# Performance work log

Measured on AMD Instinct MI355X. Metric: run time of the kernel, lower is better.

Reference implementation:

```python
import jax, jax.numpy as jnp
import numpy as np

N = 50000
E = 600000
F_IN = 256
H = 128            # num_hidden_units * num_heads (heads=1)
C = 20             # num_classes
NEG_SLOPE = 0.2    # PyG GATConv default


def setup_inputs() -> dict:
    key = jax.random.key(0)
    ks = jax.random.split(key, 16)
    g = lambda k, shape, fan: jax.random.normal(k, shape, jnp.float32) / np.sqrt(fan)
    return {
        "x": jax.random.normal(ks[0], (N, F_IN), jnp.float32),
        "edge_index": jax.random.randint(ks[1], (2, E), 0, N, jnp.int64),
        # GATConv 1: F_IN -> H (heads=1, concat)
        "W1": g(ks[2], (F_IN, H), F_IN),
        "a_src1": g(ks[3], (H,), H),
        "a_dst1": g(ks[4], (H,), H),
        "b1": jnp.zeros((H,), jnp.float32),
        # GATConv 2: H -> H (heads=1)
        "W2": g(ks[5], (H, H), H),
        "a_src2": g(ks[6], (H,), H),
        "a_dst2": g(ks[7], (H,), H),
        "b2": jnp.zeros((H,), jnp.float32),
        # MLP head
        "Wm1": g(ks[8], (H, H), H),
        "bm1": jnp.zeros((H,), jnp.float32),
        "Wm2": g(ks[9], (H, C), H),
        "bm2": jnp.zeros((C,), jnp.float32),
    }


def gat_layer(x, W, a_src, a_dst, b, src, dst, n_nodes):
    """Single-head GATConv (PyG semantics, self-loops already in src/dst)."""
    h = x @ W                                    # [N, H]
    # edge attention logits: leaky_relu(a_src . h_j + a_dst . h_i)
    logits = jax.nn.leaky_relu((h @ a_src)[src] + (h @ a_dst)[dst], NEG_SLOPE)  # [Etot]
    # softmax over incoming edges per target node
    m = jax.ops.segment_max(logits, dst, num_segments=n_nodes)
    e = jnp.exp(logits - m[dst])
    denom = jax.ops.segment_sum(e, dst, num_segments=n_nodes)
    coef = e / denom[dst]                        # [Etot]
    out = jax.ops.segment_sum(coef[:, None] * h[src], dst, num_segments=n_nodes)
    return out + b


def reference(x, edge_index, W1, a_src1, a_dst1, b1, W2, a_src2, a_dst2, b2, Wm1, bm1, Wm2, bm2):
    n = x.shape[0]
    loops = jnp.arange(n, dtype=edge_index.dtype)
    src = jnp.concatenate([edge_index[0], loops])  # add self loops (GATConv default)
    dst = jnp.concatenate([edge_index[1], loops])
    h = gat_layer(x, W1, a_src1, a_dst1, b1, src, dst, n)
    h = jax.nn.relu(h)                            # dropout = identity at eval
    h = gat_layer(h, W2, a_src2, a_dst2, b2, src, dst, n)
    # MLP head: Linear -> (dropout) -> ReLU -> Linear -> sigmoid
    z = jax.nn.relu(h @ Wm1 + bm1)
    return jax.nn.sigmoid(z @ Wm2 + bm2)
```

## Files before the change

kernel.cpp:

```cpp
#include <hip/hip_runtime.h>
#include <math.h>

#define F_IN 256
#define HDIM 128
#define NCLS 20
#define NEG_SLOPE 0.2f
#define SCAN_CHUNK 1024

typedef float f32x4 __attribute__((ext_vector_type(4)));
typedef _Float16 f16x2 __attribute__((ext_vector_type(2)));
typedef _Float16 f16x4 __attribute__((ext_vector_type(4)));
typedef _Float16 f16x8 __attribute__((ext_vector_type(8)));

static __device__ __forceinline__ float lrelu(float x) { return x > 0.f ? x : NEG_SLOPE * x; }

__global__ void count_kernel(const int* __restrict__ ei, int E, int N, int* __restrict__ deg) {
    int e = blockIdx.x * blockDim.x + threadIdx.x;
    int Etot = E + N;
    if (e >= Etot) return;
    int d = (e < E) ? ei[E + e] : (e - E);
    atomicAdd(&deg[d], 1);
}

__global__ __launch_bounds__(256) void scan_reduce_kernel(const int* __restrict__ deg, int n,
                                                          int* __restrict__ bsums) {
    int base = blockIdx.x * SCAN_CHUNK + threadIdx.x * 4;
    int s = 0;
    if (base + 3 < n) {
        int4 v = *reinterpret_cast<const int4*>(&deg[base]);
        s = v.x + v.y + v.z + v.w;
    } else {
#pragma unroll
        for (int j = 0; j < 4; ++j) if (base + j < n) s += deg[base + j];
    }
#pragma unroll
    for (int o = 32; o > 0; o >>= 1) s += __shfl_down(s, o);
    __shared__ int ws[4];
    int lane = threadIdx.x & 63, w = threadIdx.x >> 6;
    if (lane == 0) ws[w] = s;
    __syncthreads();
    if (threadIdx.x == 0) bsums[blockIdx.x] = ws[0] + ws[1] + ws[2] + ws[3];
}

__global__ __launch_bounds__(256) void scan_bsums_kernel(int* __restrict__ bsums, int nb,
                                                         int* __restrict__ off, int n) {
    __shared__ int sh[256];
    int tid = threadIdx.x;
    int v = (tid < nb) ? bsums[tid] : 0;
    sh[tid] = v;
    __syncthreads();
    for (int d = 1; d < 256; d <<= 1) {
        int t = (tid >= d) ? sh[tid - d] : 0;
        __syncthreads();
        sh[tid] += t;
        __syncthreads();
    }
    if (tid < nb) bsums[tid] = sh[tid] - v;
    if (tid == 255) off[n] = sh[255];
}

__global__ __launch_bounds__(256) void scan_down_kernel(const int* __restrict__ deg, int n,
                                                        const int* __restrict__ bpre,
                                                        int* __restrict__ off) {
    int base = blockIdx.x * SCAN_CHUNK + threadIdx.x * 4;
    int v0 = 0, v1 = 0, v2 = 0, v3 = 0;
    if (base + 3 < n) {
        int4 t = *reinterpret_cast<const int4*>(&deg[base]);
        v0 = t.x; v1 = t.y; v2 = t.z; v3 = t.w;
    } else {
        if (base + 0 < n) v0 = deg[base + 0];
        if (base + 1 < n) v1 = deg[base + 1];
        if (base + 2 < n) v2 = deg[base + 2];
        if (base + 3 < n) v3 = deg[base + 3];
    }
    int tsum = v0 + v1 + v2 + v3;
    int lane = threadIdx.x & 63, w = threadIdx.x >> 6;
    int inc = tsum;
#pragma unroll
    for (int o = 1; o < 64; o <<= 1) {
        int t = __shfl_up(inc, o);
        if (lane >= o) inc += t;
    }
    int texc = inc - tsum;
    __shared__ int wsum[4];
    if (lane == 63) wsum[w] = inc;
    __syncthreads();
    int wpre = 0;
    for (int i = 0; i < w; ++i) wpre += wsum[i];
    int p = bpre[blockIdx.x] + wpre + texc;
    if (base + 3 < n) {
        int4 o4;
        o4.x = p; o4.y = p + v0; o4.z = p + v0 + v1; o4.w = p + v0 + v1 + v2;
        *reinterpret_cast<int4*>(&off[base]) = o4;
    } else {
        int run = p;
        if (base + 0 < n) { off[base + 0] = run; run += v0; }
        if (base + 1 < n) { off[base + 1] = run; run += v1; }
        if (base + 2 < n) { off[base + 2] = run; run += v2; }
        if (base + 3 < n) { off[base + 3] = run; }
    }
}

__global__ void scatter_kernel(const int* __restrict__ ei, int E, int N,
                               const int* __restrict__ off, int* __restrict__ cursor,
                               int* __restrict__ csr_src) {
    int e = blockIdx.x * blockDim.x + threadIdx.x;
    int Etot = E + N;
    if (e >= Etot) return;
    int s, d;
    if (e < E) { s = ei[e]; d = ei[E + e]; } else { s = d = e - E; }
    int pos = off[d] + atomicAdd(&cursor[d], 1);
    csr_src[pos] = s;
}

__global__ __launch_bounds__(64) void pack_b_kernel(const float* __restrict__ W1,
                                                    const float* __restrict__ W2,
                                                    const float* __restrict__ Wm1,
                                                    _Float16* __restrict__ p1,
                                                    _Float16* __restrict__ p2,
                                                    _Float16* __restrict__ p3) {
    int t = blockIdx.x;
    int lane = threadIdx.x;
    const float* B; _Float16* out; int r;
    if (t < 64)      { B = W1;  out = p1; r = t; }
    else if (t < 96) { B = W2;  out = p2; r = t - 64; }
    else             { B = Wm1; out = p3; r = t - 96; }
    int ks = r >> 3, cf = r & 7;
    int c  = cf * 16 + (lane & 15);
    int k0 = ks * 32 + (lane >> 4) * 8;
    size_t base = ((size_t)r * 64 + lane) * 16;
#pragma unroll
    for (int i = 0; i < 8; ++i) {
        float v = B[(size_t)(k0 + i) * 128 + c];
        _Float16 h = (_Float16)v;
        out[base + i]     = h;
        out[base + 8 + i] = (_Float16)(v - (float)h);
    }
}

template <int AFMT, int KSTEPS>
__global__ __launch_bounds__(256) void gemm_mfma_kernel(
        const void* __restrict__ Aptr, const _Float16* __restrict__ Bp,
        _Float16* __restrict__ C, int M,
        const float* __restrict__ bias, int act,
        const float* __restrict__ a_src, const float* __restrict__ a_dst,
        float* __restrict__ as_out, float* __restrict__ ad_out) {
    constexpr int K = KSTEPS * 32;
    __shared__ float sal[2][2][64];

    int tid = threadIdx.x;
    int lane = tid & 63;
    int wid = tid >> 6;
    int wr = wid >> 1, wc = wid & 1;
    int bm = blockIdx.x * 64;
    int l15 = lane & 15, l4 = lane >> 4;
    int row0 = bm + wr * 32 + l15;
    int koff = l4 * 8;

    const float*    A32 = (const float*)Aptr;
    const _Float16* A16 = (const _Float16*)Aptr;
    bool ok0 = row0 < M, ok1 = (row0 + 16) < M;
    const f16x8 zf = {0, 0, 0, 0, 0, 0, 0, 0};

    f32x4 acc[2][4];
#pragma unroll
    for (int m = 0; m < 2; ++m)
#pragma unroll
        for (int j = 0; j < 4; ++j) acc[m][j] = (f32x4){0.f, 0.f, 0.f, 0.f};

    auto loadA = [&](int ks, f16x8 a[2]) {
        int kb = ks * 32 + koff;
#pragma unroll
        for (int m = 0; m < 2; ++m) {
            int rr = row0 + m * 16;
            bool ok = m ? ok1 : ok0;
            if (AFMT == 0) {
                if (ok) {
                    const float* p = &A32[(size_t)rr * K + kb];
                    float4 u = *reinterpret_cast<const float4*>(p);
                    float4 w = *reinterpret_cast<const float4*>(p + 4);
                    f16x8 t;
                    t[0] = (_Float16)u.x; t[1] = (_Float16)u.y;
                    t[2] = (_Float16)u.z; t[3] = (_Float16)u.w;
                    t[4] = (_Float16)w.x; t[5] = (_Float16)w.y;
                    t[6] = (_Float16)w.z; t[7] = (_Float16)w.w;
                    a[m] = t;
                } else a[m] = zf;
            } else {
                a[m] = ok ? *reinterpret_cast<const f16x8*>(&A16[(size_t)rr * K + kb]) : zf;
            }
        }
    };
    auto loadB = [&](int ks, f16x8 bh[4], f16x8 bl[4]) {
#pragma unroll
        for (int j = 0; j < 4; ++j) {
            int cf = wc * 4 + j;
            const _Float16* p = Bp + (((size_t)ks * 8 + cf) * 64 + lane) * 16;
            bh[j] = *reinterpret_cast<const f16x8*>(p);
            bl[j] = *reinterpret_cast<const f16x8*>(p + 8);
        }
    };

    f16x8 a0[2], a1[2], bh0[4], bh1[4], bl0[4], bl1[4];
    loadA(0, a0); loadB(0, bh0, bl0);
#pragma unroll
    for (int ks = 0; ks < KSTEPS; ks += 2) {
        loadA(ks + 1, a1); loadB(ks + 1, bh1, bl1);
#pragma unroll
        for (int j = 0; j < 4; ++j) {
            acc[0][j] = __builtin_amdgcn_mfma_f32_16x16x32_f16(a0[0], bh0[j], acc[0][j], 0, 0, 0);
            acc[1][j] = __builtin_amdgcn_mfma_f32_16x16x32_f16(a0[1], bh0[j], acc[1][j], 0, 0, 0);
            acc[0][j] = __builtin_amdgcn_mfma_f32_16x16x32_f16(a0[0], bl0[j], acc[0][j], 0, 0, 0);
            acc[1][j] = __builtin_amdgcn_mfma_f32_16x16x32_f16(a0[1], bl0[j], acc[1][j], 0, 0, 0);
        }
        if (ks + 2 < KSTEPS) { loadA(ks + 2, a0); loadB(ks + 2, bh0, bl0); }
#pragma unroll
        for (int j = 0; j < 4; ++j) {
            acc[0][j] = __builtin_amdgcn_mfma_f32_16x16x32_f16(a1[0], bh1[j], acc[0][j], 0, 0, 0);
            acc[1][j] = __builtin_amdgcn_mfma_f32_16x16x32_f16(a1[1], bh1[j], acc[1][j], 0, 0, 0);
            acc[0][j] = __builtin_amdgcn_mfma_f32_16x16x32_f16(a1[0], bl1[j], acc[0][j], 0, 0, 0);
            acc[1][j] = __builtin_amdgcn_mfma_f32_16x16x32_f16(a1[1], bl1[j], acc[1][j], 0, 0, 0);
        }
    }

    float ps[2][4], pd[2][4];
#pragma unroll
    for (int m = 0; m < 2; ++m)
#pragma unroll
        for (int reg = 0; reg < 4; ++reg) { ps[m][reg] = 0.f; pd[m][reg] = 0.f; }

#pragma unroll
    for (int j = 0; j < 4; ++j) {
        int col = wc * 64 + j * 16 + l15;
        float bi = bias ? bias[col] : 0.f;
        float asc = a_src ? a_src[col] : 0.f;
        float adc = a_src ? a_dst[col] : 0.f;
#pragma unroll
        for (int m = 0; m < 2; ++m) {
#pragma unroll
            for (int reg = 0; reg < 4; ++reg) {
                int rr = bm + wr * 32 + m * 16 + l4 * 4 + reg;
                float v = acc[m][j][reg] + bi;
                if (act) v = fmaxf(v, 0.f);
                if (rr < M) C[(size_t)rr * 128 + col] = (_Float16)v;
                ps[m][reg] = fmaf(v, asc, ps[m][reg]);
                pd[m][reg] = fmaf(v, adc, pd[m][reg]);
            }
        }
    }

    if (a_src) {
#pragma unroll
        for (int o = 1; o < 16; o <<= 1) {
#pragma unroll
            for (int m = 0; m < 2; ++m)
#pragma unroll
                for (int reg = 0; reg < 4; ++reg) {
                    ps[m][reg] += __shfl_xor(ps[m][reg], o);
                    pd[m][reg] += __shfl_xor(pd[m][reg], o);
                }
        }
        if (l15 == 0) {
#pragma unroll
            for (int m = 0; m < 2; ++m)
#pragma unroll
                for (int reg = 0; reg < 4; ++reg) {
                    int rloc = wr * 32 + m * 16 + l4 * 4 + reg;
                    sal[0][wc][rloc] = ps[m][reg];
                    sal[1][wc][rloc] = pd[m][reg];
                }
        }
        __syncthreads();
        if (tid < 64) {
            int rr = bm + tid;
            if (rr < M) {
                as_out[rr] = sal[0][0][tid] + sal[0][1][tid];
                ad_out[rr] = sal[1][0][tid] + sal[1][1][tid];
            }
        }
    }
}

__global__ __launch_bounds__(256) void aggregate_kernel(const _Float16* __restrict__ h,
                                 const float* __restrict__ asrc, const float* __restrict__ adst,
                                 const int* __restrict__ off, const int* __restrict__ csr_src,
                                 const float* __restrict__ bias,
                                 _Float16* __restrict__ out,
                                 int N, int do_relu) {
    __shared__ float2 sm[4][64];
    int wslot = threadIdx.x >> 6;
    int wave = blockIdx.x * 4 + wslot;
    int lane = threadIdx.x & 63;
    if (wave >= N) return;
    int o0 = off[wave], o1 = off[wave + 1];
    float ad = adst[wave];
    int l31 = lane & 31;
    int jst = lane >> 5;

    float denom = 0.f;
    float4 aA = make_float4(0.f, 0.f, 0.f, 0.f);
    float4 aB = make_float4(0.f, 0.f, 0.f, 0.f);

    for (int base = o0; base < o1; base += 64) {
        int cnt = o1 - base; if (cnt > 64) cnt = 64;
        float e = 0.f; int s = 0;
        if (lane < cnt) {
            s = csr_src[base + lane];
            e = __expf(lrelu(asrc[s] + ad));
        }
        float t = e;
#pragma unroll
        for (int o = 32; o > 0; o >>= 1) t += __shfl_xor(t, o);
        denom += t;
        sm[wslot][lane] = make_float2(__int_as_float(s), e);

        int j = jst;
        for (; j + 2 < cnt; j += 4) {
            float2 s0 = sm[wslot][j];
            float2 s1 = sm[wslot][j + 2];
            f16x4 h0 = *reinterpret_cast<const f16x4*>(&h[(size_t)__float_as_int(s0.x) * HDIM + 4 * l31]);
            f16x4 h1 = *reinterpret_cast<const f16x4*>(&h[(size_t)__float_as_int(s1.x) * HDIM + 4 * l31]);
            aA.x = fmaf(s0.y, (float)h0[0], aA.x);
            aA.y = fmaf(s0.y, (float)h0[1], aA.y);
            aA.z = fmaf(s0.y, (float)h0[2], aA.z);
            aA.w = fmaf(s0.y, (float)h0[3], aA.w);
            aB.x = fmaf(s1.y, (float)h1[0], aB.x);
            aB.y = fmaf(s1.y, (float)h1[1], aB.y);
            aB.z = fmaf(s1.y, (float)h1[2], aB.z);
            aB.w = fmaf(s1.y, (float)h1[3], aB.w);
        }
        if (j < cnt) {
            float2 s0 = sm[wslot][j];
            f16x4 h0 = *reinterpret_cast<const f16x4*>(&h[(size_t)__float_as_int(s0.x) * HDIM + 4 * l31]);
            aA.x = fmaf(s0.y, (float)h0[0], aA.x);
            aA.y = fmaf(s0.y, (float)h0[1], aA.y);
            aA.z = fmaf(s0.y, (float)h0[2], aA.z);
            aA.w = fmaf(s0.y, (float)h0[3], aA.w);
        }
    }

    aA.x += aB.x; aA.y += aB.y; aA.z += aB.z; aA.w += aB.w;
    aA.x += __shfl_xor(aA.x, 32);
    aA.y += __shfl_xor(aA.y, 32);
    aA.z += __shfl_xor(aA.z, 32);
    aA.w += __shfl_xor(aA.w, 32);

    if (lane < 32) {
        float inv = 1.f / denom;
        float4 bi = *reinterpret_cast<const float4*>(&bias[4 * l31]);
        float v0 = aA.x * inv + bi.x;
        float v1 = aA.y * inv + bi.y;
        float v2 = aA.z * inv + bi.z;
        float v3 = aA.w * inv + bi.w;
        if (do_relu) {
            v0 = fmaxf(v0, 0.f); v1 = fmaxf(v1, 0.f);
            v2 = fmaxf(v2, 0.f); v3 = fmaxf(v3, 0.f);
        }
        f16x4 o4;
        o4[0] = (_Float16)v0; o4[1] = (_Float16)v1;
        o4[2] = (_Float16)v2; o4[3] = (_Float16)v3;
        *reinterpret_cast<f16x4*>(&out[(size_t)wave * HDIM + 4 * l31]) = o4;
    }
}

__global__ __launch_bounds__(256) void head_kernel(const _Float16* __restrict__ Z,
                                                   const float* __restrict__ W,
                                                   const float* __restrict__ b,
                                                   float* __restrict__ out, int N) {
    __shared__ float Ws[HDIM][NCLS];
    __shared__ float Zs[256][33];
    int tid = threadIdx.x;
    for (int i = tid; i < HDIM * NCLS; i += 256) Ws[i / NCLS][i % NCLS] = W[i];
    float acc[NCLS];
#pragma unroll
    for (int c = 0; c < NCLS; ++c) acc[c] = 0.f;
    int row = blockIdx.x * 256 + tid;
    for (int k0 = 0; k0 < HDIM; k0 += 32) {
        __syncthreads();
#pragma unroll
        for (int t = 0; t < 8; ++t) {
            int flat = tid * 4 + t * 1024;
            int r = flat >> 5, kk = flat & 31;
            int gr = blockIdx.x * 256 + r;
            if (gr < N) {
                f16x4 v = *reinterpret_cast<const f16x4*>(&Z[(size_t)gr * HDIM + k0 + kk]);
                Zs[r][kk] = (float)v[0]; Zs[r][kk + 1] = (float)v[1];
                Zs[r][kk + 2] = (float)v[2]; Zs[r][kk + 3] = (float)v[3];
            } else {
                Zs[r][kk] = 0.f; Zs[r][kk + 1] = 0.f; Zs[r][kk + 2] = 0.f; Zs[r][kk + 3] = 0.f;
            }
        }
        __syncthreads();
#pragma unroll
        for (int kk = 0; kk < 32; ++kk) {
            float a = Zs[tid][kk];
#pragma unroll
            for (int c = 0; c < NCLS; ++c) acc[c] = fmaf(a, Ws[k0 + kk][c], acc[c]);
        }
    }
    if (row < N) {
#pragma unroll
        for (int c = 0; c < NCLS; ++c) {
            float v = acc[c] + b[c];
            out[(size_t)row * NCLS + c] = 1.f / (1.f + expf(-v));
        }
    }
}

extern "C" void kernel_launch(void* const* d_in, const int* in_sizes, int n_in,
                              void* d_out, int out_size, void* d_ws, size_t ws_size,
                              hipStream_t stream) {
    const float* x      = (const float*)d_in[0];
    const int*   ei     = (const int*)d_in[1];
    const float* W1     = (const float*)d_in[2];
    const float* a_src1 = (const float*)d_in[3];
    const float* a_dst1 = (const float*)d_in[4];
    const float* b1     = (const float*)d_in[5];
    const float* W2     = (const float*)d_in[6];
    const float* a_src2 = (const float*)d_in[7];
    const float* a_dst2 = (const float*)d_in[8];
    const float* b2     = (const float*)d_in[9];
    const float* Wm1    = (const float*)d_in[10];
    const float* bm1    = (const float*)d_in[11];
    const float* Wm2    = (const float*)d_in[12];
    const float* bm2    = (const float*)d_in[13];

    int N = in_sizes[0] / F_IN;
    int E = in_sizes[1] / 2;
    int Etot = E + N;

    char* ws = (char*)d_ws;
    size_t pos = 0;
    auto alloc = [&](size_t bytes) -> void* {
        void* p = ws + pos;
        pos = (pos + bytes + 255) & ~(size_t)255;
        return p;
    };
    _Float16* h16 = (_Float16*)alloc((size_t)N * HDIM * 2);
    _Float16* f16 = (_Float16*)alloc((size_t)N * HDIM * 2);
    float* as_buf = (float*)alloc((size_t)N * 4);
    float* ad_buf = (float*)alloc((size_t)N * 4);
    int*   deg    = (int*)alloc((size_t)N * 4);
    int*   offs   = (int*)alloc((size_t)(N + 1) * 4);
    int*   cursor = (int*)alloc((size_t)N * 4);
    int*   csr    = (int*)alloc((size_t)Etot * 4);
    int*   bsums  = (int*)alloc(256 * 4);
    _Float16* p1 = (_Float16*)alloc(65536 * 2);
    _Float16* p2 = (_Float16*)alloc(32768 * 2);
    _Float16* p3 = (_Float16*)alloc(32768 * 2);

    hipMemsetAsync(deg, 0, (size_t)N * 4, stream);
    hipMemsetAsync(cursor, 0, (size_t)N * 4, stream);

    int eb = (Etot + 255) / 256;
    int nb = (N + SCAN_CHUNK - 1) / SCAN_CHUNK;
    count_kernel<<<eb, 256, 0, stream>>>(ei, E, N, deg);
    scan_reduce_kernel<<<nb, 256, 0, stream>>>(deg, N, bsums);
    scan_bsums_kernel<<<1, 256, 0, stream>>>(bsums, nb, offs, N);
    scan_down_kernel<<<nb, 256, 0, stream>>>(deg, N, bsums, offs);
    scatter_kernel<<<eb, 256, 0, stream>>>(ei, E, N, offs, cursor, csr);

    pack_b_kernel<<<128, 64, 0, stream>>>(W1, W2, Wm1, p1, p2, p3);

    int gemm_blocks = (N + 63) / 64;
    int wave_blocks = (N + 3) / 4;

    gemm_mfma_kernel<0, 8><<<gemm_blocks, 256, 0, stream>>>(x, p1, h16, N, nullptr, 0,
                                                            a_src1, a_dst1, as_buf, ad_buf);
    aggregate_kernel<<<wave_blocks, 256, 0, stream>>>(h16, as_buf, ad_buf, offs, csr, b1, f16, N, 1);

    gemm_mfma_kernel<1, 4><<<gemm_blocks, 256, 0, stream>>>(f16, p2, h16, N, nullptr, 0,
                                                            a_src2, a_dst2, as_buf, ad_buf);
    aggregate_kernel<<<wave_blocks, 256, 0, stream>>>(h16, as_buf, ad_buf, offs, csr, b2, f16, N, 0);

    gemm_mfma_kernel<1, 4><<<gemm_blocks, 256, 0, stream>>>(f16, p3, h16, N, bm1, 1,
                                                            nullptr, nullptr, nullptr, nullptr);
    head_kernel<<<(N + 255) / 256, 256, 0, stream>>>(h16, Wm2, bm2, (float*)d_out, N);
}
```

Measured before the change: 225.4 us.

## Fuse MLP output head into final GEMM and split GEMM across eight waves

The final Linear+sigmoid head is computed inside the third MFMA GEMM: activated rows are staged in shared memory in fp32 and each block computes its 64x20 outputs there, which removes the separate head kernel and the fp16 round-trip of the hidden activations through global memory. All GEMMs now use 512-thread blocks with 8 waves, each wave covering 32 output columns instead of 64, which raises wave count per block and lowers per-wave accumulator registers. The trade-off is more shared memory in the fused variant, A-tile loads duplicated across four column waves, and an extra sync before the head.

```diff
diff --git a/kernel.cpp b/kernel.cpp
--- a/kernel.cpp
+++ b/kernel.cpp
@@ -138,35 +138,45 @@
     }
 }
 
-template <int AFMT, int KSTEPS>
-__global__ __launch_bounds__(256) void gemm_mfma_kernel(
+template <int AFMT, int KSTEPS, int FUSE_HEAD>
+__global__ __launch_bounds__(512) void gemm_mfma_kernel(
         const void* __restrict__ Aptr, const _Float16* __restrict__ Bp,
         _Float16* __restrict__ C, int M,
         const float* __restrict__ bias, int act,
         const float* __restrict__ a_src, const float* __restrict__ a_dst,
-        float* __restrict__ as_out, float* __restrict__ ad_out) {
+        float* __restrict__ as_out, float* __restrict__ ad_out,
+        const float* __restrict__ Wh, const float* __restrict__ bh2,
+        float* __restrict__ outp) {
     constexpr int K = KSTEPS * 32;
-    __shared__ float sal[2][2][64];
+    __shared__ float sal[2][4][64];
+    __shared__ float zs[FUSE_HEAD ? 64 : 1][FUSE_HEAD ? 132 : 1];
+    __shared__ float Wt[FUSE_HEAD ? 20 : 1][FUSE_HEAD ? 132 : 1];
+    __shared__ float bb[FUSE_HEAD ? 20 : 1];
 
     int tid = threadIdx.x;
     int lane = tid & 63;
     int wid = tid >> 6;
-    int wr = wid >> 1, wc = wid & 1;
+    int wr = wid >> 2, wc = wid & 3;
     int bm = blockIdx.x * 64;
     int l15 = lane & 15, l4 = lane >> 4;
     int row0 = bm + wr * 32 + l15;
     int koff = l4 * 8;
 
+    if constexpr (FUSE_HEAD) {
+        for (int i = tid; i < HDIM * NCLS; i += 512) Wt[i % NCLS][i / NCLS] = Wh[i];
+        if (tid < NCLS) bb[tid] = bh2[tid];
+    }
+
     const float*    A32 = (const float*)Aptr;
     const _Float16* A16 = (const _Float16*)Aptr;
     bool ok0 = row0 < M, ok1 = (row0 + 16) < M;
     const f16x8 zf = {0, 0, 0, 0, 0, 0, 0, 0};
 
-    f32x4 acc[2][4];
+    f32x4 acc[2][2];
 #pragma unroll
     for (int m = 0; m < 2; ++m)
 #pragma unroll
-        for (int j = 0; j < 4; ++j) acc[m][j] = (f32x4){0.f, 0.f, 0.f, 0.f};
+        for (int j = 0; j < 2; ++j) acc[m][j] = (f32x4){0.f, 0.f, 0.f, 0.f};
 
     auto loadA = [&](int ks, f16x8 a[2]) {
         int kb = ks * 32 + koff;
@@ -191,23 +201,23 @@
             }
         }
     };
-    auto loadB = [&](int ks, f16x8 bh[4], f16x8 bl[4]) {
-#pragma unroll
-        for (int j = 0; j < 4; ++j) {
-            int cf = wc * 4 + j;
+    auto loadB = [&](int ks, f16x8 bh[2], f16x8 bl[2]) {
+#pragma unroll
+        for (int j = 0; j < 2; ++j) {
+            int cf = wc * 2 + j;
             const _Float16* p = Bp + (((size_t)ks * 8 + cf) * 64 + lane) * 16;
             bh[j] = *reinterpret_cast<const f16x8*>(p);
             bl[j] = *reinterpret_cast<const f16x8*>(p + 8);
         }
     };
 
-    f16x8 a0[2], a1[2], bh0[4], bh1[4], bl0[4], bl1[4];
+    f16x8 a0[2], a1[2], bh0[2], bh1[2], bl0[2], bl1[2];
     loadA(0, a0); loadB(0, bh0, bl0);
 #pragma unroll
     for (int ks = 0; ks < KSTEPS; ks += 2) {
         loadA(ks + 1, a1); loadB(ks + 1, bh1, bl1);
 #pragma unroll
-        for (int j = 0; j < 4; ++j) {
+        for (int j = 0; j < 2; ++j) {
             acc[0][j] = __builtin_amdgcn_mfma_f32_16x16x32_f16(a0[0], bh0[j], acc[0][j], 0, 0, 0);
             acc[1][j] = __builtin_amdgcn_mfma_f32_16x16x32_f16(a0[1], bh0[j], acc[1][j], 0, 0, 0);
             acc[0][j] = __builtin_amdgcn_mfma_f32_16x16x32_f16(a0[0], bl0[j], acc[0][j], 0, 0, 0);
@@ -215,7 +225,7 @@
         }
         if (ks + 2 < KSTEPS) { loadA(ks + 2, a0); loadB(ks + 2, bh0, bl0); }
 #pragma unroll
-        for (int j = 0; j < 4; ++j) {
+        for (int j = 0; j < 2; ++j) {
             acc[0][j] = __builtin_amdgcn_mfma_f32_16x16x32_f16(a1[0], bh1[j], acc[0][j], 0, 0, 0);
             acc[1][j] = __builtin_amdgcn_mfma_f32_16x16x32_f16(a1[1], bh1[j], acc[1][j], 0, 0, 0);
             acc[0][j] = __builtin_amdgcn_mfma_f32_16x16x32_f16(a1[0], bl1[j], acc[0][j], 0, 0, 0);
@@ -230,8 +240,8 @@
         for (int reg = 0; reg < 4; ++reg) { ps[m][reg] = 0.f; pd[m][reg] = 0.f; }
 
 #pragma unroll
-    for (int j = 0; j < 4; ++j) {
-        int col = wc * 64 + j * 16 + l15;
+    for (int j = 0; j < 2; ++j) {
+        int col = wc * 32 + j * 16 + l15;
         float bi = bias ? bias[col] : 0.f;
         float asc = a_src ? a_src[col] : 0.f;
         float adc = a_src ? a_dst[col] : 0.f;
@@ -239,10 +249,15 @@
         for (int m = 0; m < 2; ++m) {
 #pragma unroll
             for (int reg = 0; reg < 4; ++reg) {
-                int rr = bm + wr * 32 + m * 16 + l4 * 4 + reg;
+                int rloc = wr * 32 + m * 16 + l4 * 4 + reg;
+                int rr = bm + rloc;
                 float v = acc[m][j][reg] + bi;
                 if (act) v = fmaxf(v, 0.f);
-                if (rr < M) C[(size_t)rr * 128 + col] = (_Float16)v;
+                if constexpr (FUSE_HEAD) {
+                    zs[rloc][col] = v;
+                } else {
+                    if (rr < M) C[(size_t)rr * 128 + col] = (_Float16)v;
+                }
                 ps[m][reg] = fmaf(v, asc, ps[m][reg]);
                 pd[m][reg] = fmaf(v, adc, pd[m][reg]);
             }
@@ -274,9 +289,29 @@
         if (tid < 64) {
             int rr = bm + tid;
             if (rr < M) {
-                as_out[rr] = sal[0][0][tid] + sal[0][1][tid];
-                ad_out[rr] = sal[1][0][tid] + sal[1][1][tid];
+                as_out[rr] = sal[0][0][tid] + sal[0][1][tid] + sal[0][2][tid] + sal[0][3][tid];
+                ad_out[rr] = sal[1][0][tid] + sal[1][1][tid] + sal[1][2][tid] + sal[1][3][tid];
             }
+        }
+    }
+
+    if constexpr (FUSE_HEAD) {
+        __syncthreads();
+        for (int idx = tid; idx < 64 * NCLS; idx += 512) {
+            int r = idx / NCLS, c = idx % NCLS;
+            int rr = bm + r;
+            if (rr >= M) continue;
+            float s = bb[c];
+#pragma unroll
+            for (int k = 0; k < HDIM; k += 4) {
+                float4 z4 = *reinterpret_cast<const float4*>(&zs[r][k]);
+                float4 w4 = *reinterpret_cast<const float4*>(&Wt[c][k]);
+                s = fmaf(z4.x, w4.x, s);
+                s = fmaf(z4.y, w4.y, s);
+                s = fmaf(z4.z, w4.z, s);
+                s = fmaf(z4.w, w4.w, s);
+            }
+            outp[(size_t)rr * NCLS + c] = 1.f / (1.f + __expf(-s));
         }
     }
 }
@@ -360,50 +395,6 @@
         o4[0] = (_Float16)v0; o4[1] = (_Float16)v1;
         o4[2] = (_Float16)v2; o4[3] = (_Float16)v3;
         *reinterpret_cast<f16x4*>(&out[(size_t)wave * HDIM + 4 * l31]) = o4;
-    }
-}
-
-__global__ __launch_bounds__(256) void head_kernel(const _Float16* __restrict__ Z,
-                                                   const float* __restrict__ W,
-                                                   const float* __restrict__ b,
-                                                   float* __restrict__ out, int N) {
-    __shared__ float Ws[HDIM][NCLS];
-    __shared__ float Zs[256][33];
-    int tid = threadIdx.x;
-    for (int i = tid; i < HDIM * NCLS; i += 256) Ws[i / NCLS][i % NCLS] = W[i];
-    float acc[NCLS];
-#pragma unroll
-    for (int c = 0; c < NCLS; ++c) acc[c] = 0.f;
-    int row = blockIdx.x * 256 + tid;
-    for (int k0 = 0; k0 < HDIM; k0 += 32) {
-        __syncthreads();
-#pragma unroll
-        for (int t = 0; t < 8; ++t) {
-            int flat = tid * 4 + t * 1024;
-            int r = flat >> 5, kk = flat & 31;
-            int gr = blockIdx.x * 256 + r;
-            if (gr < N) {
-                f16x4 v = *reinterpret_cast<const f16x4*>(&Z[(size_t)gr * HDIM + k0 + kk]);
-                Zs[r][kk] = (float)v[0]; Zs[r][kk + 1] = (float)v[1];
-                Zs[r][kk + 2] = (float)v[2]; Zs[r][kk + 3] = (float)v[3];
-            } else {
-                Zs[r][kk] = 0.f; Zs[r][kk + 1] = 0.f; Zs[r][kk + 2] = 0.f; Zs[r][kk + 3] = 0.f;
-            }
-        }
-        __syncthreads();
-#pragma unroll
-        for (int kk = 0; kk < 32; ++kk) {
-            float a = Zs[tid][kk];
-#pragma unroll
-            for (int c = 0; c < NCLS; ++c) acc[c] = fmaf(a, Ws[k0 + kk][c], acc[c]);
-        }
-    }
-    if (row < N) {
-#pragma unroll
-        for (int c = 0; c < NCLS; ++c) {
-            float v = acc[c] + b[c];
-            out[(size_t)row * NCLS + c] = 1.f / (1.f + expf(-v));
-        }
     }
 }
 
@@ -465,15 +456,17 @@
     int gemm_blocks = (N + 63) / 64;
     int wave_blocks = (N + 3) / 4;
 
-    gemm_mfma_kernel<0, 8><<<gemm_blocks, 256, 0, stream>>>(x, p1, h16, N, nullptr, 0,
-                                                            a_src1, a_dst1, as_buf, ad_buf);
+    gemm_mfma_kernel<0, 8, 0><<<gemm_blocks, 512, 0, stream>>>(x, p1, h16, N, nullptr, 0,
+                                                               a_src1, a_dst1, as_buf, ad_buf,
+                                                               nullptr, nullptr, nullptr);
     aggregate_kernel<<<wave_blocks, 256, 0, stream>>>(h16, as_buf, ad_buf, offs, csr, b1, f16, N, 1);
 
-    gemm_mfma_kernel<1, 4><<<gemm_blocks, 256, 0, stream>>>(f16, p2, h16, N, nullptr, 0,
-                                                            a_src2, a_dst2, as_buf, ad_buf);
+    gemm_mfma_kernel<1, 4, 0><<<gemm_blocks, 512, 0, stream>>>(f16, p2, h16, N, nullptr, 0,
+                                                               a_src2, a_dst2, as_buf, ad_buf,
+                                                               nullptr, nullptr, nullptr);
     aggregate_kernel<<<wave_blocks, 256, 0, stream>>>(h16, as_buf, ad_buf, offs, csr, b2, f16, N, 0);
 
-    gemm_mfma_kernel<1, 4><<<gemm_blocks, 256, 0, stream>>>(f16, p3, h16, N, bm1, 1,
-                                                            nullptr, nullptr, nullptr, nullptr);
-    head_kernel<<<(N + 255) / 256, 256, 0, stream>>>(h16, Wm2, bm2, (float*)d_out, N);
-}
+    gemm_mfma_kernel<1, 4, 1><<<gemm_blocks, 512, 0, stream>>>(f16, p3, h16, N, bm1, 1,
+                                                               nullptr, nullptr, nullptr, nullptr,
+                                                               Wm2, bm2, (float*)d_out);
+}
```

New measurement: 227.3 us. About the same (+0.8%).
